# Kernel tuning notes

Hardware: AMD Instinct MI355X
Metric: run time of the kernel (lower is better)

## Reference

```python
import math
import jax, jax.numpy as jnp
import numpy as np

B, S, HID = 2, 2048, 2048
H, D = 32, 64  # num heads, head dim (H*D == HID)


def setup_inputs() -> dict:
    key = jax.random.key(0)
    ks = jax.random.split(key, 5)
    scale = 1.0 / math.sqrt(HID)
    return {
        "hidden_states": jax.random.normal(ks[0], (B, S, HID), dtype=jnp.float32),
        "attention_mask": jnp.zeros((B, S), dtype=jnp.float32),
        "wq": jax.random.normal(ks[1], (HID, HID), dtype=jnp.float32) * scale,
        "wk": jax.random.normal(ks[2], (HID, HID), dtype=jnp.float32) * scale,
        "wv": jax.random.normal(ks[3], (HID, HID), dtype=jnp.float32) * scale,
        "wo": jax.random.normal(ks[4], (HID, HID), dtype=jnp.float32) * scale,
    }


def reference(hidden_states, attention_mask, wq, wk, wv, wo):
    b, s, _ = hidden_states.shape
    # QKV projections (nn.Linear stores weight as [out, in]; y = x @ W^T)
    q = (hidden_states @ wq.T).reshape(b, s, H, D).transpose(0, 2, 1, 3)  # [B,H,S,D]
    k = (hidden_states @ wk.T).reshape(b, s, H, D).transpose(0, 2, 1, 3)
    v = (hidden_states @ wv.T).reshape(b, s, H, D).transpose(0, 2, 1, 3)
    # rotary_emb_ is None in the source module, so no RoPE is applied.
    scores = jnp.einsum("bhqd,bhkd->bhqk", q, k) / math.sqrt(D)  # [B,H,S,S]
    scores = scores + attention_mask.reshape(b, 1, 1, s)  # additive mask
    probs = jax.nn.softmax(scores, axis=-1)
    ctx = jnp.einsum("bhqk,bhkd->bhqd", probs, v)  # [B,H,S,D]
    ctx = ctx.transpose(0, 2, 1, 3).reshape(b, s, H * D)  # [B,S,HID]
    return ctx @ wo.T
```

## Files before the change

### kernel.cpp

```cpp
#include <hip/hip_runtime.h>

using bf16x8 = __attribute__((ext_vector_type(8))) __bf16;
using f32x4  = __attribute__((ext_vector_type(4))) float;
using uint2v = __attribute__((ext_vector_type(2))) unsigned int;

__device__ __forceinline__ unsigned short f2bf(float x) {
  unsigned int u = __float_as_uint(x);
  u += 0x7fffu + ((u >> 16) & 1u);
  return (unsigned short)(u >> 16);
}

__device__ __forceinline__ void gload16(const unsigned short* g, unsigned short* l) {
  __builtin_amdgcn_global_load_lds(
      (__attribute__((address_space(1))) void*)const_cast<unsigned short*>(g),
      (__attribute__((address_space(3))) void*)l, 16, 0, 0);
}

__global__ __launch_bounds__(256) void cvt_kernel(const float* __restrict__ in,
                                                  unsigned short* __restrict__ out) {
  const int i = blockIdx.x * 256 + threadIdx.x;
  const float4 v = ((const float4*)in)[i];
  ushort4 o;
  o.x = f2bf(v.x); o.y = f2bf(v.y); o.z = f2bf(v.z); o.w = f2bf(v.w);
  ((ushort4*)out)[i] = o;
}

template<int MODE>
__global__ __launch_bounds__(512, 1)
void gemm3(const unsigned short* __restrict__ A,
           const unsigned short* __restrict__ Bw,
           float* __restrict__ Cf,
           unsigned short* __restrict__ Cq,
           int M, int N, int K)
{
  __shared__ unsigned short Sh[3 * 24576];
  const int tid  = threadIdx.x;
  const int lane = tid & 63;
  const int wid  = tid >> 6;
  const int wm   = wid >> 2;
  const int wn   = wid & 3;
  const int lrow = lane & 15, lhi = lane >> 4;

  const int gY   = gridDim.y;
  const int nwg  = gridDim.x * gY;
  const int flat = blockIdx.x * gY + blockIdx.y;
  const int swzb = (flat & 7) * (nwg >> 3) + (flat >> 3);
  const int bn   = (swzb / gY) * 256;
  const int bm   = (swzb % gY) * 128;

  const int NT = K >> 6;

  const int srow = tid >> 3;
  const int sswz = (((tid & 7) ^ (srow & 7)) << 3);
  const unsigned short* AgS = A  + (size_t)(bm + srow) * K + sswz;
  const unsigned short* BgS = Bw + (size_t)(bn + srow) * K + sswz;

  auto stage = [&](int t, unsigned short* base) {
    const unsigned short* ag = AgS + (size_t)t * 64;
    const unsigned short* bg = BgS + (size_t)t * 64;
    gload16(ag,                   base + tid * 8);
    gload16(ag + (size_t)64 * K,  base + 4096  + tid * 8);
    gload16(bg,                   base + 8192  + tid * 8);
    gload16(bg + (size_t)64 * K,  base + 12288 + tid * 8);
    gload16(bg + (size_t)128 * K, base + 16384 + tid * 8);
    gload16(bg + (size_t)192 * K, base + 20480 + tid * 8);
  };

  int aoff[4], boff[4], coff[2];
#pragma unroll
  for (int m = 0; m < 4; ++m) aoff[m] = (wm * 64 + m * 16 + lrow) * 64;
#pragma unroll
  for (int n = 0; n < 4; ++n) boff[n] = 8192 + (wn * 64 + n * 16 + lrow) * 64;
  coff[0] = ((lhi)     ^ (lrow & 7)) << 3;
  coff[1] = ((lhi + 4) ^ (lrow & 7)) << 3;

  f32x4 acc[4][4] = {};

  stage(0, Sh);
  stage(1, Sh + 24576);
  asm volatile("s_waitcnt vmcnt(6)" ::: "memory");
  __builtin_amdgcn_s_barrier();

  int cb = 0;
  for (int t = 0; t < NT; ++t) {
    if (t + 2 < NT) {
      int sb = cb + 2; if (sb >= 3) sb -= 3;
      stage(t + 2, Sh + sb * 24576);
    }
    const unsigned short* crd = Sh + cb * 24576;
    bf16x8 a_[2][4], b_[2][4];
#pragma unroll
    for (int ks = 0; ks < 2; ++ks) {
#pragma unroll
      for (int m = 0; m < 4; ++m) a_[ks][m] = *(const bf16x8*)(crd + aoff[m] + coff[ks]);
#pragma unroll
      for (int n = 0; n < 4; ++n) b_[ks][n] = *(const bf16x8*)(crd + boff[n] + coff[ks]);
    }
    __builtin_amdgcn_s_setprio(1);
#pragma unroll
    for (int ks = 0; ks < 2; ++ks)
#pragma unroll
      for (int m = 0; m < 4; ++m)
#pragma unroll
        for (int n = 0; n < 4; ++n)
          acc[m][n] = __builtin_amdgcn_mfma_f32_16x16x32_bf16(a_[ks][m], b_[ks][n], acc[m][n], 0, 0, 0);
    __builtin_amdgcn_s_setprio(0);
    if (t + 2 < NT) {
      asm volatile("s_waitcnt vmcnt(6)" ::: "memory");
      __builtin_amdgcn_s_barrier();
    } else if (t + 1 < NT) {
      asm volatile("s_waitcnt vmcnt(0)" ::: "memory");
      __builtin_amdgcn_s_barrier();
    }
    cb = (cb + 1 == 3) ? 0 : cb + 1;
  }

#pragma unroll
  for (int m = 0; m < 4; ++m) {
    const int row0 = bm + wm * 64 + m * 16 + lhi * 4;
#pragma unroll
    for (int n = 0; n < 4; ++n) {
      const int col = bn + wn * 64 + n * 16 + lrow;
#pragma unroll
      for (int r = 0; r < 4; ++r) {
        const int row = row0 + r;
        const float v = acc[m][n][r];
        if (MODE == 0) {
          const int which = col >> 11;
          const int h = (col >> 6) & 31;
          const int d = col & 63;
          const int b = row >> 11;
          const int s = row & 2047;
          if (which == 2) {
            Cq[(size_t)16777216 + ((size_t)(b * 32 + h) * 64 + d) * 2048 + s] = f2bf(v);
          } else {
            Cq[(((size_t)which * 64 + b * 32 + h) * 2048 + s) * 64 + d] = f2bf(v);
          }
        } else {
          Cf[(size_t)row * N + col] = v;
        }
      }
    }
  }
}

__global__ __launch_bounds__(256)
void attn_kernel(const unsigned short* __restrict__ QKV,
                 const float* __restrict__ mask,
                 unsigned short* __restrict__ Ctx)
{
  constexpr int S = 2048, D = 64, BH = 64;
  __shared__ unsigned short Klds[2][64 * 64];
  __shared__ unsigned short Vlds[2][64 * 64];
  __shared__ unsigned short PT[4][64 * 16];

  const int tid  = threadIdx.x;
  const int lane = tid & 63;
  const int wid  = tid >> 6;
  const int lrow = lane & 15;
  const int lhi  = lane >> 4;
  const int bh = blockIdx.y;
  const int b  = bh >> 5;
  const int h  = bh & 31;
  const int qbase = blockIdx.x * 64;

  const size_t qoff = (size_t)bh * S * D;
  const size_t koff = qoff + (size_t)BH * S * D;
  const size_t voff = koff + (size_t)BH * S * D;

  bf16x8 qa0, qa1;
  {
    const unsigned short* Qp = QKV + qoff + (size_t)(qbase + wid * 16 + lrow) * D + lhi * 8;
    qa0 = *(const bf16x8*)Qp;
    qa1 = *(const bf16x8*)(Qp + 32);
  }

  f32x4 oacc[4] = {};
  float srow[4] = {0.f, 0.f, 0.f, 0.f};

  const int strow  = tid >> 3;
  const int sswz   = ((tid & 7) ^ (strow & 7)) << 3;
  const unsigned short* Kg = QKV + koff + (size_t)strow * D + sswz;
  const unsigned short* Vg = QKV + voff + (size_t)strow * S + sswz;

  const float k1 = 0.125f * 1.44269504f;
  const unsigned ptbase =
      (unsigned)(uintptr_t)&PT[wid][0] + (unsigned)(lane * 8 + (lane >> 4) * 128);

  auto stage = [&](int t, int c) {
    const int kb = t * 64;
    gload16(Kg + (size_t)kb * D,          &Klds[c][0] + tid * 8);
    gload16(Kg + (size_t)kb * D + 32 * D, &Klds[c][0] + 2048 + tid * 8);
    gload16(Vg + kb,                      &Vlds[c][0] + tid * 8);
    gload16(Vg + kb + 32 * S,             &Vlds[c][0] + 2048 + tid * 8);
  };

  stage(0, 0);
  __syncthreads();

  for (int t = 0; t < S / 64; ++t) {
    const int kb  = t * 64;
    const int cur = t & 1;
    if (t + 1 < S / 64) stage(t + 1, cur ^ 1);

    float mkl[4];
#pragma unroll
    for (int f = 0; f < 4; ++f)
      mkl[f] = mask[(size_t)b * S + kb + lrow + 16 * f] * 1.44269504f;

    const unsigned short* Kc = &Klds[cur][0];
    f32x4 sacc[4] = {};
#pragma unroll
    for (int f = 0; f < 4; ++f) {
      const int krw = f * 16 + lrow;
      bf16x8 kf0 = *(const bf16x8*)(Kc + krw * 64 + ((lhi ^ (lrow & 7)) << 3));
      bf16x8 kf1 = *(const bf16x8*)(Kc + krw * 64 + (((lhi + 4) ^ (lrow & 7)) << 3));
      sacc[f] = __builtin_amdgcn_mfma_f32_16x16x32_bf16(qa0, kf0, sacc[f], 0, 0, 0);
      sacc[f] = __builtin_amdgcn_mfma_f32_16x16x32_bf16(qa1, kf1, sacc[f], 0, 0, 0);
    }

#pragma unroll
    for (int f = 0; f < 4; ++f)
#pragma unroll
      for (int r = 0; r < 4; ++r) {
        const float p = __builtin_amdgcn_exp2f(sacc[f][r] * k1 + mkl[f]);
        sacc[f][r] = p;
        srow[r] += p;
      }

    unsigned short* PTw = &PT[wid][0];
#pragma unroll
    for (int f = 0; f < 4; ++f) {
      unsigned w0, w1;
      asm("v_cvt_pk_bf16_f32 %0, %1, %2" : "=v"(w0) : "v"(sacc[f][0]), "v"(sacc[f][1]));
      asm("v_cvt_pk_bf16_f32 %0, %1, %2" : "=v"(w1) : "v"(sacc[f][2]), "v"(sacc[f][3]));
      uint2v w; w.x = w0; w.y = w1;
      *(uint2v*)(PTw + (lrow + 16 * f) * 16 + lhi * 4) = w;
    }

    const unsigned short* Vc = &Vlds[cur][0];
    uint2v r0, r1, r2, r3;
    asm volatile("ds_read_b64_tr_b16 %0, %1"             : "=v"(r0) : "v"(ptbase) : "memory");
    asm volatile("ds_read_b64_tr_b16 %0, %1 offset:128"  : "=v"(r1) : "v"(ptbase) : "memory");
    asm volatile("ds_read_b64_tr_b16 %0, %1 offset:1024" : "=v"(r2) : "v"(ptbase) : "memory");
    asm volatile("ds_read_b64_tr_b16 %0, %1 offset:1152" : "=v"(r3) : "v"(ptbase) : "memory");
    bf16x8 vb[2][4];
#pragma unroll
    for (int ks = 0; ks < 2; ++ks)
#pragma unroll
      for (int f = 0; f < 4; ++f) {
        const int dc = lrow + 16 * f;
        vb[ks][f] = *(const bf16x8*)(Vc + dc * 64 + (((ks * 4 + lhi) ^ (dc & 7)) << 3));
      }
    asm volatile("s_waitcnt lgkmcnt(0)" ::: "memory");
    __builtin_amdgcn_sched_barrier(0);
    union { struct { uint2v a, b; } u; bf16x8 v; } p0, p1;
    p0.u.a = r0; p0.u.b = r1;
    p1.u.a = r2; p1.u.b = r3;
#pragma unroll
    for (int f = 0; f < 4; ++f)
      oacc[f] = __builtin_amdgcn_mfma_f32_16x16x32_bf16(p0.v, vb[0][f], oacc[f], 0, 0, 0);
#pragma unroll
    for (int f = 0; f < 4; ++f)
      oacc[f] = __builtin_amdgcn_mfma_f32_16x16x32_bf16(p1.v, vb[1][f], oacc[f], 0, 0, 0);
    __syncthreads();
  }

#pragma unroll
  for (int off = 1; off < 16; off <<= 1)
#pragma unroll
    for (int r = 0; r < 4; ++r)
      srow[r] += __shfl_xor(srow[r], off, 64);

#pragma unroll
  for (int f = 0; f < 4; ++f) {
    const int d = lrow + 16 * f;
#pragma unroll
    for (int r = 0; r < 4; ++r) {
      const int q = qbase + wid * 16 + lhi * 4 + r;
      const float v = oacc[f][r] / srow[r];
      Ctx[((size_t)b * S + q) * 2048 + h * 64 + d] = f2bf(v);
    }
  }
}

extern "C" void kernel_launch(void* const* d_in, const int* in_sizes, int n_in,
                              void* d_out, int out_size, void* d_ws, size_t ws_size,
                              hipStream_t stream) {
  const float* X    = (const float*)d_in[0];
  const float* mask = (const float*)d_in[1];
  const float* wq   = (const float*)d_in[2];
  const float* wk   = (const float*)d_in[3];
  const float* wv   = (const float*)d_in[4];
  const float* wo   = (const float*)d_in[5];

  unsigned short* ws   = (unsigned short*)d_ws;
  unsigned short* Xb   = ws;
  unsigned short* Wcat = Xb + 8388608;
  unsigned short* Wob  = Wcat + 12582912;
  unsigned short* QKVb = Wob + 4194304;
  unsigned short* Ctxb = QKVb + 25165824;

  cvt_kernel<<<8192, 256, 0, stream>>>(X, Xb);
  cvt_kernel<<<4096, 256, 0, stream>>>(wq, Wcat);
  cvt_kernel<<<4096, 256, 0, stream>>>(wk, Wcat + 4194304);
  cvt_kernel<<<4096, 256, 0, stream>>>(wv, Wcat + 8388608);
  cvt_kernel<<<4096, 256, 0, stream>>>(wo, Wob);

  gemm3<0><<<dim3(24, 32), 512, 0, stream>>>(Xb, Wcat, nullptr, QKVb, 4096, 6144, 2048);

  attn_kernel<<<dim3(32, 64), 256, 0, stream>>>(QKVb, mask, Ctxb);

  gemm3<1><<<dim3(8, 32), 512, 0, stream>>>(Ctxb, Wob, (float*)d_out, nullptr, 4096, 2048, 2048);
}
```

Baseline: 456.2 us.

## Use 256x256 GEMM tiles with 4-phase ping-pong schedule; row sums via MFMA

The GEMM moves from 128x256 tiles with a triple-buffered LDS pipeline to 256x256 tiles. It double-buffers LDS and splits each K-step into four quadrant phases, each interleaving LDS fragment reads, the next tile's global-to-LDS loads and barriers. This aims to raise arithmetic intensity and overlap loads with MFMA, at the cost of more barriers, more accumulator registers and fewer workgroups in the grid (384 and 128). In attention, the softmax denominator is now accumulated with an extra MFMA against a ones vector rather than scalar adds and a final shuffle reduction, and MFMA sections get raised priority.

```diff
diff --git a/kernel.cpp b/kernel.cpp
--- a/kernel.cpp
+++ b/kernel.cpp
@@ -25,15 +25,35 @@
   ((ushort4*)out)[i] = o;
 }
 
+#define LOADA(mh) { _Pragma("unroll") for (int mf = 0; mf < 4; ++mf) { \
+    const int row_ = wm * 128 + (mh) * 64 + mf * 16 + lrow; \
+    af[mf][0] = *(const bf16x8*)(cb + row_ * 64 + ((lhi ^ (lrow & 7)) << 3)); \
+    af[mf][1] = *(const bf16x8*)(cb + row_ * 64 + (((lhi + 4) ^ (lrow & 7)) << 3)); } }
+#define LOADB(nh) { _Pragma("unroll") for (int nf = 0; nf < 2; ++nf) { \
+    const int row_ = wn * 64 + (nh) * 32 + nf * 16 + lrow; \
+    bfr[nf][0] = *(const bf16x8*)(cb + 16384 + row_ * 64 + ((lhi ^ (lrow & 7)) << 3)); \
+    bfr[nf][1] = *(const bf16x8*)(cb + 16384 + row_ * 64 + (((lhi + 4) ^ (lrow & 7)) << 3)); } }
+#define MMAQ(mh, nh) { \
+    __builtin_amdgcn_s_setprio(1); \
+    _Pragma("unroll") for (int mf = 0; mf < 4; ++mf) \
+      _Pragma("unroll") for (int nf = 0; nf < 2; ++nf) \
+        _Pragma("unroll") for (int ks = 0; ks < 2; ++ks) \
+          acc[(mh) * 4 + mf][(nh) * 2 + nf] = __builtin_amdgcn_mfma_f32_16x16x32_bf16( \
+              af[mf][ks], bfr[nf][ks], acc[(mh) * 4 + mf][(nh) * 2 + nf], 0, 0, 0); \
+    __builtin_amdgcn_s_setprio(0); }
+#define PHASE_SYNC_PRE() { __builtin_amdgcn_s_barrier(); \
+    asm volatile("s_waitcnt lgkmcnt(0)" ::: "memory"); \
+    __builtin_amdgcn_sched_barrier(0); }
+
 template<int MODE>
-__global__ __launch_bounds__(512, 1)
-void gemm3(const unsigned short* __restrict__ A,
-           const unsigned short* __restrict__ Bw,
-           float* __restrict__ Cf,
-           unsigned short* __restrict__ Cq,
-           int M, int N, int K)
+__global__ __launch_bounds__(512, 2)
+void gemm256(const unsigned short* __restrict__ A,
+             const unsigned short* __restrict__ Bw,
+             float* __restrict__ Cf,
+             unsigned short* __restrict__ Cq,
+             int M, int N, int K)
 {
-  __shared__ unsigned short Sh[3 * 24576];
+  __shared__ unsigned short Sh[2][32768];
   const int tid  = threadIdx.x;
   const int lane = tid & 63;
   const int wid  = tid >> 6;
@@ -46,85 +66,74 @@
   const int flat = blockIdx.x * gY + blockIdx.y;
   const int swzb = (flat & 7) * (nwg >> 3) + (flat >> 3);
   const int bn   = (swzb / gY) * 256;
-  const int bm   = (swzb % gY) * 128;
-
-  const int NT = K >> 6;
+  const int bm   = (swzb % gY) * 256;
+  const int NT   = K >> 6;
 
   const int srow = tid >> 3;
-  const int sswz = (((tid & 7) ^ (srow & 7)) << 3);
+  const int sswz = ((tid & 7) ^ (srow & 7)) << 3;
   const unsigned short* AgS = A  + (size_t)(bm + srow) * K + sswz;
   const unsigned short* BgS = Bw + (size_t)(bn + srow) * K + sswz;
 
-  auto stage = [&](int t, unsigned short* base) {
-    const unsigned short* ag = AgS + (size_t)t * 64;
-    const unsigned short* bg = BgS + (size_t)t * 64;
-    gload16(ag,                   base + tid * 8);
-    gload16(ag + (size_t)64 * K,  base + 4096  + tid * 8);
-    gload16(bg,                   base + 8192  + tid * 8);
-    gload16(bg + (size_t)64 * K,  base + 12288 + tid * 8);
-    gload16(bg + (size_t)128 * K, base + 16384 + tid * 8);
-    gload16(bg + (size_t)192 * K, base + 20480 + tid * 8);
-  };
-
-  int aoff[4], boff[4], coff[2];
-#pragma unroll
-  for (int m = 0; m < 4; ++m) aoff[m] = (wm * 64 + m * 16 + lrow) * 64;
-#pragma unroll
-  for (int n = 0; n < 4; ++n) boff[n] = 8192 + (wn * 64 + n * 16 + lrow) * 64;
-  coff[0] = ((lhi)     ^ (lrow & 7)) << 3;
-  coff[1] = ((lhi + 4) ^ (lrow & 7)) << 3;
-
-  f32x4 acc[4][4] = {};
-
-  stage(0, Sh);
-  stage(1, Sh + 24576);
-  asm volatile("s_waitcnt vmcnt(6)" ::: "memory");
+  f32x4  acc[8][4] = {};
+  bf16x8 af[4][2], bfr[2][2];
+
+  gload16(AgS,                   &Sh[0][0] + tid * 8);
+  gload16(AgS + (size_t)64  * K, &Sh[0][0] + 4096  + tid * 8);
+  gload16(AgS + (size_t)128 * K, &Sh[0][0] + 8192  + tid * 8);
+  gload16(AgS + (size_t)192 * K, &Sh[0][0] + 12288 + tid * 8);
+  gload16(BgS,                   &Sh[0][0] + 16384 + tid * 8);
+  gload16(BgS + (size_t)64  * K, &Sh[0][0] + 20480 + tid * 8);
+  gload16(BgS + (size_t)128 * K, &Sh[0][0] + 24576 + tid * 8);
+  gload16(BgS + (size_t)192 * K, &Sh[0][0] + 28672 + tid * 8);
+  asm volatile("s_waitcnt vmcnt(0)" ::: "memory");
   __builtin_amdgcn_s_barrier();
 
-  int cb = 0;
   for (int t = 0; t < NT; ++t) {
-    if (t + 2 < NT) {
-      int sb = cb + 2; if (sb >= 3) sb -= 3;
-      stage(t + 2, Sh + sb * 24576);
-    }
-    const unsigned short* crd = Sh + cb * 24576;
-    bf16x8 a_[2][4], b_[2][4];
-#pragma unroll
-    for (int ks = 0; ks < 2; ++ks) {
-#pragma unroll
-      for (int m = 0; m < 4; ++m) a_[ks][m] = *(const bf16x8*)(crd + aoff[m] + coff[ks]);
-#pragma unroll
-      for (int n = 0; n < 4; ++n) b_[ks][n] = *(const bf16x8*)(crd + boff[n] + coff[ks]);
-    }
-    __builtin_amdgcn_s_setprio(1);
-#pragma unroll
-    for (int ks = 0; ks < 2; ++ks)
-#pragma unroll
-      for (int m = 0; m < 4; ++m)
-#pragma unroll
-        for (int n = 0; n < 4; ++n)
-          acc[m][n] = __builtin_amdgcn_mfma_f32_16x16x32_bf16(a_[ks][m], b_[ks][n], acc[m][n], 0, 0, 0);
-    __builtin_amdgcn_s_setprio(0);
-    if (t + 2 < NT) {
-      asm volatile("s_waitcnt vmcnt(6)" ::: "memory");
-      __builtin_amdgcn_s_barrier();
-    } else if (t + 1 < NT) {
-      asm volatile("s_waitcnt vmcnt(0)" ::: "memory");
-      __builtin_amdgcn_s_barrier();
-    }
-    cb = (cb + 1 == 3) ? 0 : cb + 1;
-  }
-
-#pragma unroll
-  for (int m = 0; m < 4; ++m) {
-    const int row0 = bm + wm * 64 + m * 16 + lhi * 4;
-#pragma unroll
-    for (int n = 0; n < 4; ++n) {
-      const int col = bn + wn * 64 + n * 16 + lrow;
+    const unsigned short* cb = &Sh[t & 1][0];
+    unsigned short* nb = &Sh[(t + 1) & 1][0];
+    const unsigned short* agn = AgS + (size_t)(t + 1) * 64;
+    const unsigned short* bgn = BgS + (size_t)(t + 1) * 64;
+    const bool pre = (t + 1 < NT);
+
+    LOADA(0); LOADB(0);
+    if (pre) { gload16(agn, nb + tid * 8); gload16(agn + (size_t)64 * K, nb + 4096 + tid * 8); }
+    PHASE_SYNC_PRE();
+    MMAQ(0, 0);
+    __builtin_amdgcn_s_barrier();
+
+    LOADB(1);
+    if (pre) { gload16(agn + (size_t)128 * K, nb + 8192 + tid * 8);
+               gload16(agn + (size_t)192 * K, nb + 12288 + tid * 8); }
+    PHASE_SYNC_PRE();
+    MMAQ(0, 1);
+    __builtin_amdgcn_s_barrier();
+
+    LOADA(1);
+    if (pre) { gload16(bgn, nb + 16384 + tid * 8);
+               gload16(bgn + (size_t)64 * K, nb + 20480 + tid * 8); }
+    PHASE_SYNC_PRE();
+    MMAQ(1, 1);
+    __builtin_amdgcn_s_barrier();
+
+    LOADB(0);
+    if (pre) { gload16(bgn + (size_t)128 * K, nb + 24576 + tid * 8);
+               gload16(bgn + (size_t)192 * K, nb + 28672 + tid * 8); }
+    PHASE_SYNC_PRE();
+    MMAQ(1, 0);
+    asm volatile("s_waitcnt vmcnt(0)" ::: "memory");
+    __builtin_amdgcn_s_barrier();
+  }
+
+#pragma unroll
+  for (int ai = 0; ai < 8; ++ai) {
+    const int row0 = bm + wm * 128 + (ai >> 2) * 64 + (ai & 3) * 16 + lhi * 4;
+#pragma unroll
+    for (int bj = 0; bj < 4; ++bj) {
+      const int col = bn + wn * 64 + (bj >> 1) * 32 + (bj & 1) * 16 + lrow;
 #pragma unroll
       for (int r = 0; r < 4; ++r) {
         const int row = row0 + r;
-        const float v = acc[m][n][r];
+        const float v = acc[ai][bj][r];
         if (MODE == 0) {
           const int which = col >> 11;
           const int h = (col >> 6) & 31;
@@ -175,8 +184,12 @@
     qa1 = *(const bf16x8*)(Qp + 32);
   }
 
+  bf16x8 vones;
+#pragma unroll
+  for (int j = 0; j < 8; ++j) vones[j] = (__bf16)1.0f;
+
   f32x4 oacc[4] = {};
-  float srow[4] = {0.f, 0.f, 0.f, 0.f};
+  f32x4 osum = {};
 
   const int strow  = tid >> 3;
   const int sswz   = ((tid & 7) ^ (strow & 7)) << 3;
@@ -210,6 +223,7 @@
 
     const unsigned short* Kc = &Klds[cur][0];
     f32x4 sacc[4] = {};
+    __builtin_amdgcn_s_setprio(1);
 #pragma unroll
     for (int f = 0; f < 4; ++f) {
       const int krw = f * 16 + lrow;
@@ -218,15 +232,13 @@
       sacc[f] = __builtin_amdgcn_mfma_f32_16x16x32_bf16(qa0, kf0, sacc[f], 0, 0, 0);
       sacc[f] = __builtin_amdgcn_mfma_f32_16x16x32_bf16(qa1, kf1, sacc[f], 0, 0, 0);
     }
+    __builtin_amdgcn_s_setprio(0);
 
 #pragma unroll
     for (int f = 0; f < 4; ++f)
 #pragma unroll
-      for (int r = 0; r < 4; ++r) {
-        const float p = __builtin_amdgcn_exp2f(sacc[f][r] * k1 + mkl[f]);
-        sacc[f][r] = p;
-        srow[r] += p;
-      }
+      for (int r = 0; r < 4; ++r)
+        sacc[f][r] = __builtin_amdgcn_exp2f(sacc[f][r] * k1 + mkl[f]);
 
     unsigned short* PTw = &PT[wid][0];
 #pragma unroll
@@ -257,20 +269,18 @@
     union { struct { uint2v a, b; } u; bf16x8 v; } p0, p1;
     p0.u.a = r0; p0.u.b = r1;
     p1.u.a = r2; p1.u.b = r3;
+    __builtin_amdgcn_s_setprio(1);
 #pragma unroll
     for (int f = 0; f < 4; ++f)
       oacc[f] = __builtin_amdgcn_mfma_f32_16x16x32_bf16(p0.v, vb[0][f], oacc[f], 0, 0, 0);
+    osum = __builtin_amdgcn_mfma_f32_16x16x32_bf16(p0.v, vones, osum, 0, 0, 0);
 #pragma unroll
     for (int f = 0; f < 4; ++f)
       oacc[f] = __builtin_amdgcn_mfma_f32_16x16x32_bf16(p1.v, vb[1][f], oacc[f], 0, 0, 0);
+    osum = __builtin_amdgcn_mfma_f32_16x16x32_bf16(p1.v, vones, osum, 0, 0, 0);
+    __builtin_amdgcn_s_setprio(0);
     __syncthreads();
   }
-
-#pragma unroll
-  for (int off = 1; off < 16; off <<= 1)
-#pragma unroll
-    for (int r = 0; r < 4; ++r)
-      srow[r] += __shfl_xor(srow[r], off, 64);
 
 #pragma unroll
   for (int f = 0; f < 4; ++f) {
@@ -278,7 +288,7 @@
 #pragma unroll
     for (int r = 0; r < 4; ++r) {
       const int q = qbase + wid * 16 + lhi * 4 + r;
-      const float v = oacc[f][r] / srow[r];
+      const float v = oacc[f][r] / osum[r];
       Ctx[((size_t)b * S + q) * 2048 + h * 64 + d] = f2bf(v);
     }
   }
@@ -307,9 +317,9 @@
   cvt_kernel<<<4096, 256, 0, stream>>>(wv, Wcat + 8388608);
   cvt_kernel<<<4096, 256, 0, stream>>>(wo, Wob);
 
-  gemm3<0><<<dim3(24, 32), 512, 0, stream>>>(Xb, Wcat, nullptr, QKVb, 4096, 6144, 2048);
+  gemm256<0><<<dim3(24, 16), 512, 0, stream>>>(Xb, Wcat, nullptr, QKVb, 4096, 6144, 2048);
 
   attn_kernel<<<dim3(32, 64), 256, 0, stream>>>(QKVb, mask, Ctxb);
 
-  gemm3<1><<<dim3(8, 32), 512, 0, stream>>>(Ctxb, Wob, (float*)d_out, nullptr, 4096, 2048, 2048);
-}
+  gemm256<1><<<dim3(8, 16), 512, 0, stream>>>(Ctxb, Wob, (float*)d_out, nullptr, 4096, 2048, 2048);
+}
```

Result: slower. 482.3 us (+5.7%).
